# Performance work log

Measured on AMD Instinct MI355X. Metric: run time of the kernel, lower is better.

The kernel has to match this reference:

```python
import jax, jax.numpy as jnp
import numpy as np

N_NODES = 50000
N_EDGES = 800000
N_GRAPHS = 500
H = 90


def _kaiming(key, shape):
    fan_in = shape[1]
    bound = np.sqrt(6.0 / fan_in)  # kaiming_uniform with relu gain ~ sqrt(2)*sqrt(3/fan_in)
    return jax.random.uniform(key, shape, jnp.float32, -bound, bound)


def setup_inputs() -> dict:
    key = jax.random.key(0)
    ks = jax.random.split(key, 16)
    x = jax.random.normal(ks[0], (N_NODES, H), jnp.float32)
    edge_index = jax.random.randint(ks[1], (2, N_EDGES), 0, N_NODES, jnp.int64)
    batch = jnp.sort(jax.random.randint(ks[2], (N_NODES,), 0, N_GRAPHS, jnp.int64))
    params = {}
    for i, l in enumerate([1, 2, 3]):
        params[f'W{l}l'] = _kaiming(ks[3 + 2 * i], (H, H))
        params[f'b{l}l'] = jnp.zeros((H,), jnp.float32)
        params[f'W{l}r'] = _kaiming(ks[4 + 2 * i], (H, H))
    params['fc1_w'] = _kaiming(ks[10], (32, H))
    params['fc1_b'] = jnp.zeros((32,), jnp.float32)
    params['fc2_w'] = _kaiming(ks[11], (1, 32))
    params['fc2_b'] = jnp.zeros((1,), jnp.float32)
    return dict(x=x, edge_index=edge_index, batch=batch, **params)


def _sage_conv(x, src, dst, Wl, bl, Wr):
    # PyG SAGEConv: out = lin_l(mean_{j in N(i)} x_j) + lin_r(x_i)
    msg = x[src]                                                # [E, H] gather
    s = jax.ops.segment_sum(msg, dst, num_segments=N_NODES)     # [N, H]
    cnt = jax.ops.segment_sum(jnp.ones((dst.shape[0], 1), x.dtype), dst,
                              num_segments=N_NODES)
    aggr = s / jnp.maximum(cnt, 1.0)
    return aggr @ Wl.T + bl + x @ Wr.T


def reference(x, edge_index, batch,
              W1l, b1l, W1r, W2l, b2l, W2r, W3l, b3l, W3r,
              fc1_w, fc1_b, fc2_w, fc2_b):
    src, dst = edge_index[0], edge_index[1]
    h1 = jax.nn.relu(_sage_conv(x, src, dst, W1l, b1l, W1r))
    h2 = jax.nn.relu(_sage_conv(h1, src, dst, W2l, b2l, W2r))
    h3 = jax.nn.relu(_sage_conv(h2, src, dst, W3l, b3l, W3r))
    # global_mean_pool over graph ids
    gs = jax.ops.segment_sum(h3, batch, num_segments=N_GRAPHS)  # [G, H]
    gc = jax.ops.segment_sum(jnp.ones((batch.shape[0], 1), h3.dtype), batch,
                             num_segments=N_GRAPHS)
    h4 = gs / jnp.maximum(gc, 1.0)
    h4 = jax.nn.relu(h4 @ fc1_w.T + fc1_b)
    return h4 @ fc2_w.T + fc2_b                                 # [G, 1]
```

## Files before the change

### kernel.cpp

```cpp
#include <hip/hip_runtime.h>
#include <hip/hip_bf16.h>

#define N_NODES 50000
#define N_EDGES 800000
#define N_GRAPHS 500
#define H 90
#define PSTRIDE 96
#define SGROWS 8
#define NGROUPS ((N_NODES + 31) / 32)

typedef __attribute__((ext_vector_type(8))) short bf16x8;
typedef __attribute__((ext_vector_type(8))) unsigned short u16x8;
typedef __attribute__((ext_vector_type(4))) float f32x4;

__device__ __forceinline__ void pack_split(float v, unsigned short& h16, unsigned short& l16) {
    unsigned u = __float_as_uint(v);
    unsigned hi = (u + 0x7fffu + ((u >> 16) & 1u)) & 0xffff0000u;
    float lo = v - __uint_as_float(hi);
    unsigned ul = __float_as_uint(lo);
    h16 = (unsigned short)(hi >> 16);
    l16 = (unsigned short)((ul + 0x7fffu + ((ul >> 16) & 1u)) >> 16);
}
__device__ __forceinline__ unsigned short pack_hi(float v) {
    unsigned u = __float_as_uint(v);
    return (unsigned short)((u + 0x7fffu + ((u >> 16) & 1u)) >> 16);
}
__device__ __forceinline__ float bfu_lo(unsigned v) { return __uint_as_float(v << 16); }
__device__ __forceinline__ float bfu_hi(unsigned v) { return __uint_as_float(v & 0xffff0000u); }

__device__ __forceinline__ int wswz(int row, int byteInRow) {
    return (row * 192 + byteInRow) ^ ((row & 7) << 4);
}

__global__ __launch_bounds__(256) void convert_x_kernel(const float* __restrict__ x,
                                                        unsigned short* __restrict__ xh) {
    int n0 = blockIdx.x * 32;
    for (int idx = threadIdx.x; idx < 32 * PSTRIDE; idx += 256) {
        int r = idx / PSTRIDE, c = idx - r * PSTRIDE;
        int n = n0 + r;
        if (n >= N_NODES) continue;
        unsigned short h16 = 0;
        if (c < H) h16 = pack_hi(x[(size_t)n * H + c]);
        xh[(size_t)n * PSTRIDE + c] = h16;
    }
}

__global__ __launch_bounds__(256) void convert_w_kernel(const float* __restrict__ w0,
                                                        const float* __restrict__ w1,
                                                        const float* __restrict__ w2,
                                                        const float* __restrict__ w3,
                                                        const float* __restrict__ w4,
                                                        const float* __restrict__ w5,
                                                        unsigned short* __restrict__ wbuf) {
    int m = blockIdx.y;
    const float* src = (m == 0) ? w0 : (m == 1) ? w1 : (m == 2) ? w2
                     : (m == 3) ? w3 : (m == 4) ? w4 : w5;
    unsigned short* dhi = wbuf + (size_t)m * 2 * 96 * 96;
    unsigned short* dlo = dhi + 96 * 96;
    int idx = blockIdx.x * blockDim.x + threadIdx.x;
    if (idx < 96 * 96) {
        int r = idx / 96, c = idx - r * 96;
        float v = (r < H && c < H) ? src[r * H + c] : 0.0f;
        unsigned short h16, l16;
        pack_split(v, h16, l16);
        dhi[idx] = h16;
        dlo[idx] = l16;
    }
}

__global__ __launch_bounds__(256) void deg_kernel(const int* __restrict__ dst,
                                                  int* __restrict__ deg) {
    int e = blockIdx.x * blockDim.x + threadIdx.x;
    if (e < N_EDGES) atomicAdd(&deg[dst[e]], 1);
}

#define SCAN_B 512
#define NSB ((N_NODES + SCAN_B - 1) / SCAN_B)
__global__ __launch_bounds__(SCAN_B) void scan1_kernel(const int* __restrict__ deg,
                                                       int* __restrict__ rowloc,
                                                       int* __restrict__ bsum) {
    __shared__ int s[SCAN_B];
    int t = threadIdx.x;
    int i = blockIdx.x * SCAN_B + t;
    int v = (i < N_NODES) ? deg[i] : 0;
    s[t] = v;
    __syncthreads();
    for (int off = 1; off < SCAN_B; off <<= 1) {
        int u = (t >= off) ? s[t - off] : 0;
        __syncthreads();
        s[t] += u;
        __syncthreads();
    }
    if (i < N_NODES) rowloc[i] = s[t] - v;
    if (t == SCAN_B - 1) bsum[blockIdx.x] = s[t];
}

__global__ __launch_bounds__(128) void scan2_kernel(const int* __restrict__ bsum,
                                                    int* __restrict__ boff) {
    __shared__ int s[128];
    int t = threadIdx.x;
    int v = (t < NSB) ? bsum[t] : 0;
    s[t] = v;
    __syncthreads();
    for (int off = 1; off < 128; off <<= 1) {
        int u = (t >= off) ? s[t - off] : 0;
        __syncthreads();
        s[t] += u;
        __syncthreads();
    }
    boff[t] = s[t] - v;
}

__global__ __launch_bounds__(256) void scan3_kernel(const int* __restrict__ rowloc,
                                                    const int* __restrict__ boff,
                                                    int* __restrict__ rowptr) {
    int i = blockIdx.x * blockDim.x + threadIdx.x;
    if (i < N_NODES) rowptr[i] = rowloc[i] + boff[i / SCAN_B];
    else if (i == N_NODES) rowptr[i] = N_EDGES;
}

#define FCHUNKS 128
__global__ __launch_bounds__(256) void fill_part_kernel(const int* __restrict__ src,
                                                        const int* __restrict__ dst,
                                                        const int* __restrict__ rowptr,
                                                        int* __restrict__ fill,
                                                        int* __restrict__ csr) {
    const int PART_SZ = N_NODES / 8;
    const int ECH = (N_EDGES + FCHUNKS - 1) / FCHUNKS;
    int p = blockIdx.x & 7;
    int chunk = blockIdx.x >> 3;
    int e0 = chunk * ECH;
    int e1 = min(e0 + ECH, N_EDGES);
    int lo = p * PART_SZ;
    int hi = lo + PART_SZ;
    for (int e = e0 + threadIdx.x; e < e1; e += 256) {
        int d = dst[e];
        if (d >= lo && d < hi) {
            int pos = atomicAdd(&fill[d], 1);
            csr[rowptr[d] + pos] = src[e];
        }
    }
}

__global__ __launch_bounds__(256) void aggregate_kernel(const unsigned* __restrict__ xhi32,
                                                        const int* __restrict__ rowptr,
                                                        const int* __restrict__ csr,
                                                        unsigned* __restrict__ ahi32) {
    int b = blockIdx.x;
    int p = b & 7, c = b >> 3;
    int g = p + 8 * (c >> 3);
    if (g >= NGROUPS) return;
    int i = c & 7;
    int wv = threadIdx.x >> 6;
    int lane = threadIdx.x & 63;
    int n = 32 * g + 4 * i + wv;

    bool act = lane < 45;
    int L = act ? lane : 44;
    int r0 = 0, r1 = 0;
    if (n < N_NODES) { r0 = rowptr[n]; r1 = rowptr[n + 1]; }

    float a0 = 0.0f, a1 = 0.0f;
    int j = r0;
    for (; j + 15 < r1; j += 16) {
        unsigned v[16];
#pragma unroll
        for (int q = 0; q < 16; ++q) v[q] = xhi32[(size_t)csr[j + q] * 48 + L];
#pragma unroll
        for (int q = 0; q < 16; ++q) { a0 += bfu_lo(v[q]); a1 += bfu_hi(v[q]); }
    }
    for (; j + 7 < r1; j += 8) {
        unsigned v[8];
#pragma unroll
        for (int q = 0; q < 8; ++q) v[q] = xhi32[(size_t)csr[j + q] * 48 + L];
#pragma unroll
        for (int q = 0; q < 8; ++q) { a0 += bfu_lo(v[q]); a1 += bfu_hi(v[q]); }
    }
    for (; j + 3 < r1; j += 4) {
        unsigned v[4];
#pragma unroll
        for (int q = 0; q < 4; ++q) v[q] = xhi32[(size_t)csr[j + q] * 48 + L];
#pragma unroll
        for (int q = 0; q < 4; ++q) { a0 += bfu_lo(v[q]); a1 += bfu_hi(v[q]); }
    }
    for (; j < r1; ++j) {
        unsigned v = xhi32[(size_t)csr[j] * 48 + L];
        a0 += bfu_lo(v);
        a1 += bfu_hi(v);
    }

    if (n < N_NODES && lane < 48) {
        unsigned vh = 0u;
        if (act) {
            float inv = 1.0f / (float)max(r1 - r0, 1);
            unsigned short h0 = pack_hi(a0 * inv);
            unsigned short h1 = pack_hi(a1 * inv);
            vh = (unsigned)h0 | ((unsigned)h1 << 16);
        }
        ahi32[(size_t)n * 48 + lane] = vh;
    }
}

template<int MODE>
__global__ __launch_bounds__(256) void combine_kernel(
        const unsigned short* __restrict__ aghi,
        const unsigned short* __restrict__ xhi,
        const unsigned short* __restrict__ wl,
        const unsigned short* __restrict__ wr,
        const float* __restrict__ bias,
        unsigned short* __restrict__ ohi,
        const int* __restrict__ batch, float* __restrict__ gs) {
    __shared__ unsigned short sWlh[96 * 96];
    __shared__ unsigned short sWrh[96 * 96];
    __shared__ float SG[SGROWS * 96];

    const int tid = threadIdx.x;
    const int lane = tid & 63;
    const int wv = tid >> 6;
    const int nhalf = wv >> 1;
    const int hhalf = wv & 1;
    const int blk0 = blockIdx.x * 32;
    const int node0 = blk0 + nhalf * 16;
    const int col = lane & 15;
    const int kq = lane >> 4;
    const int tbase = hhalf * 3;
    const int nA = min(node0 + col, N_NODES - 1);

    bf16x8 Gh[3], Xh[3];
#pragma unroll
    for (int ks = 0; ks < 3; ++ks) {
        size_t aoff = (size_t)nA * PSTRIDE + ks * 32 + kq * 8;
        Gh[ks] = *reinterpret_cast<const bf16x8*>(aghi + aoff);
        Xh[ks] = *reinterpret_cast<const bf16x8*>(xhi + aoff);
    }

    if (MODE == 2)
        for (int i = tid; i < SGROWS * 96; i += 256) SG[i] = 0.0f;

    for (int idx = tid; idx < 96 * 12; idx += 256) {
        int r = idx / 12, c8 = idx - r * 12;
        u16x8 a = *reinterpret_cast<const u16x8*>(wl + r * 96 + c8 * 8);
        u16x8 b = *reinterpret_cast<const u16x8*>(wr + r * 96 + c8 * 8);
        *(u16x8*)((char*)sWlh + wswz(r, c8 * 16)) = a;
        *(u16x8*)((char*)sWrh + wswz(r, c8 * 16)) = b;
    }
    __syncthreads();

    float bv[3];
#pragma unroll
    for (int t = 0; t < 3; ++t) {
        int h = (tbase + t) * 16 + col;
        bv[t] = (h < H) ? bias[h] : 0.0f;
    }

    f32x4 acc[3] = {};

#pragma unroll
    for (int pass = 0; pass < 2; ++pass) {
        const unsigned short* wlo = (pass ? wr : wl) + 96 * 96;
        const unsigned short* sH = pass ? sWrh : sWlh;
#pragma unroll
        for (int ks = 0; ks < 3; ++ks) {
            const bf16x8 Ah = pass ? Xh[ks] : Gh[ks];
            const int kb = ks * 64 + kq * 16;
            bf16x8 Bh[3], Bl[3];
#pragma unroll
            for (int t = 0; t < 3; ++t) {
                int wrow = (tbase + t) * 16 + col;
                Bh[t] = *(const bf16x8*)((const char*)sH + wswz(wrow, kb));
                Bl[t] = *reinterpret_cast<const bf16x8*>(wlo + wrow * 96 + ks * 32 + kq * 8);
            }
#pragma unroll
            for (int t = 0; t < 3; ++t)
                acc[t] = __builtin_amdgcn_mfma_f32_16x16x32_bf16(Ah, Bh[t], acc[t], 0, 0, 0);
#pragma unroll
            for (int t = 0; t < 3; ++t)
                acc[t] = __builtin_amdgcn_mfma_f32_16x16x32_bf16(Ah, Bl[t], acc[t], 0, 0, 0);
        }
    }

    int gmin = 0, gnode[4];
    if (MODE == 2) {
        gmin = batch[blk0];
#pragma unroll
        for (int r = 0; r < 4; ++r) {
            int node = node0 + kq * 4 + r;
            gnode[r] = (node < N_NODES) ? batch[node] : -1;
        }
    }
#pragma unroll
    for (int t = 0; t < 3; ++t) {
        int h = (tbase + t) * 16 + col;
        if (h >= H) continue;
#pragma unroll
        for (int r = 0; r < 4; ++r) {
            int node = node0 + kq * 4 + r;
            if (node >= N_NODES) continue;
            float v = fmaxf(acc[t][r] + bv[t], 0.0f);
            if (MODE == 2) {
                int gl = gnode[r] - gmin;
                if (gl < SGROWS) atomicAdd(&SG[gl * 96 + h], v);
                else atomicAdd(&gs[gnode[r] * H + h], v);
            } else {
                ohi[(size_t)node * PSTRIDE + h] = pack_hi(v);
            }
        }
    }
    if (MODE == 2) {
        __syncthreads();
        for (int idx = tid; idx < SGROWS * 96; idx += 256) {
            int r = idx / 96, c = idx - r * 96;
            float s = SG[idx];
            if (c < H && s != 0.0f) atomicAdd(&gs[(gmin + r) * H + c], s);
        }
    }
}

__global__ __launch_bounds__(256) void pool_cnt_kernel(const int* __restrict__ batch,
                                                       float* __restrict__ gc) {
    int i = blockIdx.x * blockDim.x + threadIdx.x;
    if (i < N_NODES) atomicAdd(&gc[batch[i]], 1.0f);
}

__global__ __launch_bounds__(64) void mlp_kernel(const float* __restrict__ gs,
                                                 const float* __restrict__ gc,
                                                 const float* __restrict__ fc1_w,
                                                 const float* __restrict__ fc1_b,
                                                 const float* __restrict__ fc2_w,
                                                 const float* __restrict__ fc2_b,
                                                 float* __restrict__ out) {
    int g = blockIdx.x;
    int t = threadIdx.x;
    __shared__ float h4[H];
    float inv = 1.0f / fmaxf(gc[g], 1.0f);
    for (int k = t; k < H; k += 64) h4[k] = gs[g * H + k] * inv;
    __syncthreads();
    float v = 0.0f;
    if (t < 32) {
        float acc = fc1_b[t];
#pragma unroll 6
        for (int k = 0; k < H; ++k) acc += h4[k] * fc1_w[t * H + k];
        v = fmaxf(acc, 0.0f) * fc2_w[t];
    }
    for (int off = 16; off; off >>= 1) v += __shfl_down(v, off, 32);
    if (t == 0) out[g] = v + fc2_b[0];
}

extern "C" void kernel_launch(void* const* d_in, const int* in_sizes, int n_in,
                              void* d_out, int out_size, void* d_ws, size_t ws_size,
                              hipStream_t stream) {
    const float* x     = (const float*)d_in[0];
    const int*   ei    = (const int*)d_in[1];
    const int*   batch = (const int*)d_in[2];
    const float* W1l = (const float*)d_in[3];
    const float* b1l = (const float*)d_in[4];
    const float* W1r = (const float*)d_in[5];
    const float* W2l = (const float*)d_in[6];
    const float* b2l = (const float*)d_in[7];
    const float* W2r = (const float*)d_in[8];
    const float* W3l = (const float*)d_in[9];
    const float* b3l = (const float*)d_in[10];
    const float* W3r = (const float*)d_in[11];
    const float* fc1_w = (const float*)d_in[12];
    const float* fc1_b = (const float*)d_in[13];
    const float* fc2_w = (const float*)d_in[14];
    const float* fc2_b = (const float*)d_in[15];

    const int* src = ei;
    const int* dst = ei + N_EDGES;

    const size_t NP = (size_t)N_NODES * PSTRIDE;
    unsigned short* P0h = (unsigned short*)d_ws;
    unsigned short* P1h = P0h + NP;
    unsigned short* AGh = P1h + NP;
    int* csr    = (int*)(AGh + NP);
    int* rowptr = csr + N_EDGES;
    unsigned short* wbuf = (unsigned short*)(rowptr + N_NODES + 1);
    float* gs = (float*)(wbuf + 6 * 2 * 96 * 96);
    float* gc = gs + N_GRAPHS * H;

    int* deg    = (int*)AGh;
    int* fil    = deg + N_NODES;
    int* rowloc = fil + N_NODES;
    int* bsum   = rowloc + N_NODES;
    int* boff   = bsum + 128;

    const unsigned short* wb1l = wbuf + 0 * 2 * 96 * 96;
    const unsigned short* wb1r = wbuf + 1 * 2 * 96 * 96;
    const unsigned short* wb2l = wbuf + 2 * 2 * 96 * 96;
    const unsigned short* wb2r = wbuf + 3 * 2 * 96 * 96;
    const unsigned short* wb3l = wbuf + 4 * 2 * 96 * 96;
    const unsigned short* wb3r = wbuf + 5 * 2 * 96 * 96;

    float* out = (float*)d_out;

    const int edgeBlocks = (N_EDGES + 255) / 256;
    const int aggBlocks  = 8 * 8 * ((NGROUPS + 7) / 8);

    convert_w_kernel<<<dim3(36, 6), 256, 0, stream>>>(W1l, W1r, W2l, W2r, W3l, W3r, wbuf);
    convert_x_kernel<<<NGROUPS, 256, 0, stream>>>(x, P0h);

    hipMemsetAsync(deg, 0, 2 * N_NODES * sizeof(int), stream);
    deg_kernel<<<edgeBlocks, 256, 0, stream>>>(dst, deg);
    scan1_kernel<<<NSB, SCAN_B, 0, stream>>>(deg, rowloc, bsum);
    scan2_kernel<<<1, 128, 0, stream>>>(bsum, boff);
    scan3_kernel<<<(N_NODES + 256) / 256, 256, 0, stream>>>(rowloc, boff, rowptr);
    fill_part_kernel<<<FCHUNKS * 8, 256, 0, stream>>>(src, dst, rowptr, fil, csr);

    hipMemsetAsync(gs, 0, (N_GRAPHS * H + N_GRAPHS) * sizeof(float), stream);
    pool_cnt_kernel<<<(N_NODES + 255) / 256, 256, 0, stream>>>(batch, gc);

    aggregate_kernel<<<aggBlocks, 256, 0, stream>>>((const unsigned*)P0h, rowptr, csr,
                                                    (unsigned*)AGh);
    combine_kernel<1><<<NGROUPS, 256, 0, stream>>>(AGh, P0h, wb1l, wb1r, b1l, P1h,
                                                   nullptr, nullptr);
    aggregate_kernel<<<aggBlocks, 256, 0, stream>>>((const unsigned*)P1h, rowptr, csr,
                                                    (unsigned*)AGh);
    combine_kernel<1><<<NGROUPS, 256, 0, stream>>>(AGh, P1h, wb2l, wb2r, b2l, P0h,
                                                   nullptr, nullptr);
    aggregate_kernel<<<aggBlocks, 256, 0, stream>>>((const unsigned*)P0h, rowptr, csr,
                                                    (unsigned*)AGh);
    combine_kernel<2><<<NGROUPS, 256, 0, stream>>>(AGh, P0h, wb3l, wb3r, b3l, nullptr,
                                                   batch, gs);

    mlp_kernel<<<N_GRAPHS, 64, 0, stream>>>(gs, gc, fc1_w, fc1_b, fc2_w, fc2_b, out);
}
```

Before: 310.3 us.

## Store CSR neighbor indices as 16-bit, simplify aggregate mapping, enlarge combine blocks

```diff
diff --git a/kernel.cpp b/kernel.cpp
--- a/kernel.cpp
+++ b/kernel.cpp
@@ -7,7 +7,8 @@
 #define H 90
 #define PSTRIDE 96
 #define SGROWS 8
-#define NGROUPS ((N_NODES + 31) / 32)
+#define NG64 ((N_NODES + 63) / 64)
+#define NG32 ((N_NODES + 31) / 32)
 
 typedef __attribute__((ext_vector_type(8))) short bf16x8;
 typedef __attribute__((ext_vector_type(8))) unsigned short u16x8;
@@ -124,7 +125,7 @@
                                                         const int* __restrict__ dst,
                                                         const int* __restrict__ rowptr,
                                                         int* __restrict__ fill,
-                                                        int* __restrict__ csr) {
+                                                        unsigned short* __restrict__ csr) {
     const int PART_SZ = N_NODES / 8;
     const int ECH = (N_EDGES + FCHUNKS - 1) / FCHUNKS;
     int p = blockIdx.x & 7;
@@ -137,28 +138,22 @@
         int d = dst[e];
         if (d >= lo && d < hi) {
             int pos = atomicAdd(&fill[d], 1);
-            csr[rowptr[d] + pos] = src[e];
+            csr[rowptr[d] + pos] = (unsigned short)src[e];
         }
     }
 }
 
 __global__ __launch_bounds__(256) void aggregate_kernel(const unsigned* __restrict__ xhi32,
                                                         const int* __restrict__ rowptr,
-                                                        const int* __restrict__ csr,
+                                                        const unsigned short* __restrict__ csr,
                                                         unsigned* __restrict__ ahi32) {
-    int b = blockIdx.x;
-    int p = b & 7, c = b >> 3;
-    int g = p + 8 * (c >> 3);
-    if (g >= NGROUPS) return;
-    int i = c & 7;
     int wv = threadIdx.x >> 6;
     int lane = threadIdx.x & 63;
-    int n = 32 * g + 4 * i + wv;
+    int n = blockIdx.x * 4 + wv;
 
     bool act = lane < 45;
     int L = act ? lane : 44;
-    int r0 = 0, r1 = 0;
-    if (n < N_NODES) { r0 = rowptr[n]; r1 = rowptr[n + 1]; }
+    int r0 = rowptr[n], r1 = rowptr[n + 1];
 
     float a0 = 0.0f, a1 = 0.0f;
     int j = r0;
@@ -189,7 +184,7 @@
         a1 += bfu_hi(v);
     }
 
-    if (n < N_NODES && lane < 48) {
+    if (lane < 48) {
         unsigned vh = 0u;
         if (act) {
             float inv = 1.0f / (float)max(r1 - r0, 1);
@@ -202,7 +197,7 @@
 }
 
 template<int MODE>
-__global__ __launch_bounds__(256) void combine_kernel(
+__global__ __launch_bounds__(512) void combine_kernel(
         const unsigned short* __restrict__ aghi,
         const unsigned short* __restrict__ xhi,
         const unsigned short* __restrict__ wl,
@@ -219,7 +214,7 @@
     const int wv = tid >> 6;
     const int nhalf = wv >> 1;
     const int hhalf = wv & 1;
-    const int blk0 = blockIdx.x * 32;
+    const int blk0 = blockIdx.x * 64;
     const int node0 = blk0 + nhalf * 16;
     const int col = lane & 15;
     const int kq = lane >> 4;
@@ -235,9 +230,9 @@
     }
 
     if (MODE == 2)
-        for (int i = tid; i < SGROWS * 96; i += 256) SG[i] = 0.0f;
-
-    for (int idx = tid; idx < 96 * 12; idx += 256) {
+        for (int i = tid; i < SGROWS * 96; i += 512) SG[i] = 0.0f;
+
+    for (int idx = tid; idx < 96 * 12; idx += 512) {
         int r = idx / 12, c8 = idx - r * 12;
         u16x8 a = *reinterpret_cast<const u16x8*>(wl + r * 96 + c8 * 8);
         u16x8 b = *reinterpret_cast<const u16x8*>(wr + r * 96 + c8 * 8);
@@ -308,7 +303,7 @@
     }
     if (MODE == 2) {
         __syncthreads();
-        for (int idx = tid; idx < SGROWS * 96; idx += 256) {
+        for (int idx = tid; idx < SGROWS * 96; idx += 512) {
             int r = idx / 96, c = idx - r * 96;
             float s = SG[idx];
             if (c < H && s != 0.0f) atomicAdd(&gs[(gmin + r) * H + c], s);
@@ -373,14 +368,13 @@
     unsigned short* P0h = (unsigned short*)d_ws;
     unsigned short* P1h = P0h + NP;
     unsigned short* AGh = P1h + NP;
-    int* csr    = (int*)(AGh + NP);
-    int* rowptr = csr + N_EDGES;
+    unsigned short* csr = AGh + NP;
+    int* rowptr = (int*)(csr + N_EDGES);
     unsigned short* wbuf = (unsigned short*)(rowptr + N_NODES + 1);
     float* gs = (float*)(wbuf + 6 * 2 * 96 * 96);
     float* gc = gs + N_GRAPHS * H;
-
-    int* deg    = (int*)AGh;
-    int* fil    = deg + N_NODES;
+    int* deg  = (int*)(gc + N_GRAPHS);
+    int* fil  = deg + N_NODES;
     int* rowloc = fil + N_NODES;
     int* bsum   = rowloc + N_NODES;
     int* boff   = bsum + 128;
@@ -395,10 +389,10 @@
     float* out = (float*)d_out;
 
     const int edgeBlocks = (N_EDGES + 255) / 256;
-    const int aggBlocks  = 8 * 8 * ((NGROUPS + 7) / 8);
+    const int aggBlocks  = N_NODES / 4;
 
     convert_w_kernel<<<dim3(36, 6), 256, 0, stream>>>(W1l, W1r, W2l, W2r, W3l, W3r, wbuf);
-    convert_x_kernel<<<NGROUPS, 256, 0, stream>>>(x, P0h);
+    convert_x_kernel<<<NG32, 256, 0, stream>>>(x, P0h);
 
     hipMemsetAsync(deg, 0, 2 * N_NODES * sizeof(int), stream);
     deg_kernel<<<edgeBlocks, 256, 0, stream>>>(dst, deg);
@@ -412,16 +406,16 @@
 
     aggregate_kernel<<<aggBlocks, 256, 0, stream>>>((const unsigned*)P0h, rowptr, csr,
                                                     (unsigned*)AGh);
-    combine_kernel<1><<<NGROUPS, 256, 0, stream>>>(AGh, P0h, wb1l, wb1r, b1l, P1h,
-                                                   nullptr, nullptr);
+    combine_kernel<1><<<NG64, 512, 0, stream>>>(AGh, P0h, wb1l, wb1r, b1l, P1h,
+                                                nullptr, nullptr);
     aggregate_kernel<<<aggBlocks, 256, 0, stream>>>((const unsigned*)P1h, rowptr, csr,
                                                     (unsigned*)AGh);
-    combine_kernel<1><<<NGROUPS, 256, 0, stream>>>(AGh, P1h, wb2l, wb2r, b2l, P0h,
-                                                   nullptr, nullptr);
+    combine_kernel<1><<<NG64, 512, 0, stream>>>(AGh, P1h, wb2l, wb2r, b2l, P0h,
+                                                nullptr, nullptr);
     aggregate_kernel<<<aggBlocks, 256, 0, stream>>>((const unsigned*)P0h, rowptr, csr,
                                                     (unsigned*)AGh);
-    combine_kernel<2><<<NGROUPS, 256, 0, stream>>>(AGh, P0h, wb3l, wb3r, b3l, nullptr,
-                                                   batch, gs);
+    combine_kernel<2><<<NG64, 512, 0, stream>>>(AGh, P0h, wb3l, wb3r, b3l, nullptr,
+                                                batch, gs);
 
     mlp_kernel<<<N_GRAPHS, 64, 0, stream>>>(gs, gc, fc1_w, fc1_b, fc2_w, fc2_b, out);
 }
```

After: 316.9 us. 2.1% more time.
